# Kernel tuning notes

Hardware: AMD Instinct MI355X
Metric: run time of the kernel (lower is better)

The kernel has to match this reference:

```python
import jax, jax.numpy as jnp
import numpy as np

NUMS = 2048
DIM = 128

def setup_inputs() -> dict:
    key = jax.random.key(0)
    k1, k2 = jax.random.split(key)
    data = jax.random.normal(k1, (32, 512, DIM), dtype=jnp.float32)
    stdv = 1.0 / np.sqrt(DIM)
    weight = jax.random.uniform(k2, (NUMS, DIM), dtype=jnp.float32, minval=-stdv, maxval=stdv)
    return {"data": data, "weight": weight}

def reference(data, weight):
    b, t, d = data.shape
    nums = weight.shape[0]
    # attention scores: [b, t, nums]
    attention = jax.nn.sigmoid(jnp.einsum('btd,kd->btk', data, weight) / jnp.sqrt(jnp.asarray(d, data.dtype)))
    k_top = nums // 16 + 1  # 129
    topk_vals, _ = jax.lax.top_k(attention, k_top)  # [b, t, k_top]
    temporal_att = topk_vals.mean(axis=-1)          # [b, t]
    half = b // 2
    augment = jnp.einsum('btk,kd->btd', attention[:half], weight)  # [b//2, t, d]
    read_query = jnp.concatenate((data[:half], augment), axis=-1)  # [b//2, t, 2d]
    mem_score = 1.0 - temporal_att
    return (mem_score, read_query)
```

## Files before the change

### kernel.cpp

```cpp
#include <hip/hip_runtime.h>

typedef unsigned short u16;
typedef unsigned int u32;
typedef __attribute__((ext_vector_type(8))) short short8;
typedef __attribute__((ext_vector_type(4))) float floatx4;

#define NUMS 2048
#define DIM 128
#define ROWS_TOT 16384
#define HALF_ROWS 8192
#define KTOP 129
#define MTILE 16
#define SP 2056
#define SCALE 0.08838834764831845f

__device__ __forceinline__ u16 f2bf(float f) {
  u32 u = __builtin_bit_cast(u32, f);
  u += 0x7FFFu + ((u >> 16) & 1u);
  return (u16)(u >> 16);
}
__device__ __forceinline__ float bf2f(u32 b) {
  return __builtin_bit_cast(float, b << 16);
}

__global__ void cvt_w_k(const float* __restrict__ w, u16* __restrict__ wb,
                        u16* __restrict__ wt) {
  __shared__ u16 tile[32][33];
  const int tx = threadIdx.x, ty = threadIdx.y;
  const int x = blockIdx.x * 32 + tx;
  const int y0 = blockIdx.y * 32;
#pragma unroll
  for (int j = 0; j < 32; j += 8) {
    const u16 v = f2bf(w[(size_t)(y0 + ty + j) * DIM + x]);
    wb[(size_t)(y0 + ty + j) * DIM + x] = v;
    tile[ty + j][tx] = v;
  }
  __syncthreads();
  const int x2 = y0 + tx;
  const int y2 = blockIdx.x * 32 + ty;
#pragma unroll
  for (int j = 0; j < 32; j += 8)
    wt[(size_t)(y2 + j) * NUMS + x2] = tile[tx][ty + j];
}

__global__ __launch_bounds__(512, 4)
void fused_k(const float* __restrict__ dataF, const u16* __restrict__ wb,
             const u16* __restrict__ wt, float* __restrict__ out) {
  __shared__ u16 S[MTILE * SP];
  const int tid = threadIdx.x;
  const int r0 = blockIdx.x * MTILE;
  const int lane = tid & 63;
  const int wave = tid >> 6;
  const int m = lane & 15;
  const int quad = lane >> 4;

  short8 dfrag[4];
  {
    const float* ap = dataF + (size_t)(r0 + m) * DIM + quad * 8;
#pragma unroll
    for (int ks = 0; ks < 4; ks++) {
      const float4 x = *(const float4*)(ap + ks * 32);
      const float4 y = *(const float4*)(ap + ks * 32 + 4);
      short8 v;
      v[0] = (short)f2bf(x.x); v[1] = (short)f2bf(x.y);
      v[2] = (short)f2bf(x.z); v[3] = (short)f2bf(x.w);
      v[4] = (short)f2bf(y.x); v[5] = (short)f2bf(y.y);
      v[6] = (short)f2bf(y.z); v[7] = (short)f2bf(y.w);
      dfrag[ks] = v;
    }
  }

  u16* sbase = S + m * SP + wave * 256 + quad * 4;
#pragma unroll 4
  for (int nt = 0; nt < 16; nt++) {
    const int n0 = wave * 256 + nt * 16;
    const u16* wp = wb + (size_t)(n0 + m) * DIM + quad * 8;
    floatx4 acc = {0.f, 0.f, 0.f, 0.f};
#pragma unroll
    for (int ks = 0; ks < 4; ks++) {
      const short8 wfrag = *(const short8*)(wp + ks * 32);
      acc = __builtin_amdgcn_mfma_f32_16x16x32_bf16(wfrag, dfrag[ks], acc, 0, 0, 0);
    }
    float a0 = 1.f / (1.f + __expf(-acc[0] * SCALE));
    float a1 = 1.f / (1.f + __expf(-acc[1] * SCALE));
    float a2 = 1.f / (1.f + __expf(-acc[2] * SCALE));
    float a3 = 1.f / (1.f + __expf(-acc[3] * SCALE));
    uint2 p;
    p.x = (u32)f2bf(a0) | ((u32)f2bf(a1) << 16);
    p.y = (u32)f2bf(a2) | ((u32)f2bf(a3) << 16);
    *(uint2*)(sbase + nt * 16) = p;
  }
  __syncthreads();

  if (r0 < HALF_ROWS) {
    {
      const int row = tid >> 5;
      const int c4 = (tid & 31) << 2;
      *(float4*)(out + 16384 + (size_t)(r0 + row) * 256 + c4) =
          *(const float4*)(dataF + (size_t)(r0 + row) * DIM + c4);
    }
    const int n0 = wave * 16;
    const u16* wtp = wt + (size_t)(n0 + m) * NUMS + quad * 8;
    const u16* sp2 = S + m * SP + quad * 8;
    floatx4 acc = {0.f, 0.f, 0.f, 0.f};
#pragma unroll 8
    for (int ks = 0; ks < 64; ks++) {
      const short8 a = *(const short8*)(wtp + ks * 32);
      const short8 b = *(const short8*)(sp2 + ks * 32);
      acc = __builtin_amdgcn_mfma_f32_16x16x32_bf16(a, b, acc, 0, 0, 0);
    }
    float4 st;
    st.x = acc[0]; st.y = acc[1]; st.z = acc[2]; st.w = acc[3];
    *(float4*)(out + 16384 + (size_t)(r0 + m) * 256 + 128 + n0 + quad * 4) = st;
  }

#pragma unroll
  for (int rv = 0; rv < 2; rv++) {
    const int rr = wave * 2 + rv;
    const u16* rp = S + rr * SP + lane * 8;
    u32 x[16], xh[16];
#pragma unroll
    for (int j = 0; j < 4; j++) {
      const short8 v = *(const short8*)(rp + j * 512);
      const u32* pv = (const u32*)&v;
      x[j * 4 + 0] = pv[0]; x[j * 4 + 1] = pv[1];
      x[j * 4 + 2] = pv[2]; x[j * 4 + 3] = pv[3];
    }
#pragma unroll
    for (int i = 0; i < 16; i++) xh[i] = x[i] | 0x80008000u;

    auto cnt_ge = [&](u32 t) -> int {
      const u32 t2 = t * 0x10001u;
      int c = 0;
#pragma unroll
      for (int i = 0; i < 16; i++)
        c += __popc((xh[i] - t2) & 0x80008000u);
      return c;
    };

    int c8[8];
#pragma unroll
    for (int j = 0; j < 8; j++) c8[j] = cnt_ge(0x3F00u + (u32)j);
    u32 pk[4];
#pragma unroll
    for (int j = 0; j < 4; j++) pk[j] = (u32)c8[2 * j] | ((u32)c8[2 * j + 1] << 16);
#pragma unroll
    for (int off = 1; off < 64; off <<= 1) {
#pragma unroll
      for (int j = 0; j < 4; j++) pk[j] += __shfl_xor(pk[j], off);
    }
    int cw[8];
#pragma unroll
    for (int j = 0; j < 4; j++) {
      cw[2 * j] = (int)(pk[j] & 0xFFFFu);
      cw[2 * j + 1] = (int)(pk[j] >> 16);
    }

    u32 lo;
    int cgt;
    if (cw[0] >= KTOP && cw[7] < KTOP) {
      int idx = 0;
#pragma unroll
      for (int j = 1; j < 8; j++) idx += (cw[j] >= KTOP) ? 1 : 0;
      lo = 0x3F00u + (u32)idx;
      cgt = cw[idx + 1];
    } else {
      u32 L = 0u, H = 0x3F81u;
      while (H - L > 1u) {
        const u32 mid = (L + H) >> 1;
        int cc = cnt_ge(mid);
#pragma unroll
        for (int off = 1; off < 64; off <<= 1) cc += __shfl_xor(cc, off);
        if (cc >= KTOP) L = mid; else H = mid;
      }
      lo = L;
      int cg = cnt_ge(lo + 1);
#pragma unroll
      for (int off = 1; off < 64; off <<= 1) cg += __shfl_xor(cg, off);
      cgt = cg;
    }

    const float vstar = bf2f(lo);
    float s = 0.f;
#pragma unroll
    for (int i = 0; i < 16; i++) {
      const float v0 = bf2f(x[i] & 0xFFFFu);
      const float v1 = __builtin_bit_cast(float, x[i] & 0xFFFF0000u);
      if (v0 > vstar) s += v0;
      if (v1 > vstar) s += v1;
    }
#pragma unroll
    for (int off = 1; off < 64; off <<= 1) s += __shfl_xor(s, off);
    if (lane == 0) {
      const float mean = (s + (float)(KTOP - cgt) * vstar) * (1.f / (float)KTOP);
      out[r0 + rr] = 1.f - mean;
    }
  }
}

extern "C" void kernel_launch(void* const* d_in, const int* in_sizes, int n_in,
                              void* d_out, int out_size, void* d_ws, size_t ws_size,
                              hipStream_t stream) {
  const float* data = (const float*)d_in[0];
  const float* weight = (const float*)d_in[1];
  float* out = (float*)d_out;

  u16* wt = (u16*)d_ws;
  u16* wb = wt + NUMS * DIM;

  cvt_w_k<<<dim3(DIM / 32, NUMS / 32), dim3(32, 8), 0, stream>>>(weight, wb, wt);
  fused_k<<<dim3(ROWS_TOT / MTILE), dim3(512), 0, stream>>>(data, wb, wt, out);
}
```

Before: 161.9 us.

## Keep attention tile in registers and split second GEMM across waves

The 16x2048 bf16 attention tile is no longer staged in shared memory. Each wave keeps its 256-column slice in registers. The second GEMM is split along K across the eight waves, with partial sums combined through LDS atomics, and the transposed weight is stored with a permuted column order so that register fragments line up with MFMA operands. The top-k threshold search is reworked into a cooperative count-and-resolve loop over shared counters, and occupancy is raised to 6 blocks per EU. In exchange, it adds LDS atomics, more block-wide syncs per search step, and register pressure from the 32-word register array.

```diff
diff --git a/kernel.cpp b/kernel.cpp
--- a/kernel.cpp
+++ b/kernel.cpp
@@ -4,6 +4,7 @@
 typedef unsigned int u32;
 typedef __attribute__((ext_vector_type(8))) short short8;
 typedef __attribute__((ext_vector_type(4))) float floatx4;
+typedef __attribute__((ext_vector_type(4))) u32 u32x4;
 
 #define NUMS 2048
 #define DIM 128
@@ -11,7 +12,6 @@
 #define HALF_ROWS 8192
 #define KTOP 129
 #define MTILE 16
-#define SP 2056
 #define SCALE 0.08838834764831845f
 
 __device__ __forceinline__ u16 f2bf(float f) {
@@ -36,27 +36,48 @@
     tile[ty + j][tx] = v;
   }
   __syncthreads();
-  const int x2 = y0 + tx;
+  const int k = y0 + tx;
+  const int s = ((k >> 2) & 3) * 8 + ((k >> 4) & 1) * 4 + (k & 3);
+  const int x2p = (k & ~31) | s;
   const int y2 = blockIdx.x * 32 + ty;
 #pragma unroll
   for (int j = 0; j < 32; j += 8)
-    wt[(size_t)(y2 + j) * NUMS + x2] = tile[tx][ty + j];
-}
-
-__global__ __launch_bounds__(512, 4)
+    wt[(size_t)(y2 + j) * NUMS + x2p] = tile[tx][ty + j];
+}
+
+__global__ __launch_bounds__(512, 6)
 void fused_k(const float* __restrict__ dataF, const u16* __restrict__ wb,
              const u16* __restrict__ wt, float* __restrict__ out) {
-  __shared__ u16 S[MTILE * SP];
+  __shared__ floatx4 accb4[16 * 32];
+  __shared__ u32x4 cntb[16][8];
+  __shared__ float vbuf[16];
+  __shared__ u32 cbuf[16];
+  __shared__ u32 basebuf[16];
+  __shared__ float sumbuf[16];
+  __shared__ u32 dbuf[16];
+  __shared__ u32 donecnt;
+  float* const accb = (float*)accb4;
+
   const int tid = threadIdx.x;
   const int r0 = blockIdx.x * MTILE;
   const int lane = tid & 63;
   const int wave = tid >> 6;
   const int m = lane & 15;
   const int quad = lane >> 4;
+  const bool firstHalf = (r0 < HALF_ROWS);
+
+  if (firstHalf) accb4[tid] = (floatx4){0.f, 0.f, 0.f, 0.f};
+  if (tid < 16) {
+    sumbuf[tid] = 0.f;
+    dbuf[tid] = 0u;
+    basebuf[tid] = 0x3F00u;
+  }
+  if (tid == 16) donecnt = 0u;
+  __syncthreads();
 
   short8 dfrag[4];
   {
-    const float* ap = dataF + (size_t)(r0 + m) * DIM + quad * 8;
+    const float* ap = dataF + (r0 + m) * DIM + quad * 8;
 #pragma unroll
     for (int ks = 0; ks < 4; ks++) {
       const float4 x = *(const float4*)(ap + ks * 32);
@@ -70,131 +91,158 @@
     }
   }
 
-  u16* sbase = S + m * SP + wave * 256 + quad * 4;
-#pragma unroll 4
+  u32 patt[32];
+#pragma unroll 2
   for (int nt = 0; nt < 16; nt++) {
     const int n0 = wave * 256 + nt * 16;
-    const u16* wp = wb + (size_t)(n0 + m) * DIM + quad * 8;
+    const u16* wp = wb + (n0 + m) * DIM + quad * 8;
     floatx4 acc = {0.f, 0.f, 0.f, 0.f};
 #pragma unroll
     for (int ks = 0; ks < 4; ks++) {
       const short8 wfrag = *(const short8*)(wp + ks * 32);
       acc = __builtin_amdgcn_mfma_f32_16x16x32_bf16(wfrag, dfrag[ks], acc, 0, 0, 0);
     }
-    float a0 = 1.f / (1.f + __expf(-acc[0] * SCALE));
-    float a1 = 1.f / (1.f + __expf(-acc[1] * SCALE));
-    float a2 = 1.f / (1.f + __expf(-acc[2] * SCALE));
-    float a3 = 1.f / (1.f + __expf(-acc[3] * SCALE));
-    uint2 p;
-    p.x = (u32)f2bf(a0) | ((u32)f2bf(a1) << 16);
-    p.y = (u32)f2bf(a2) | ((u32)f2bf(a3) << 16);
-    *(uint2*)(sbase + nt * 16) = p;
-  }
-  __syncthreads();
-
-  if (r0 < HALF_ROWS) {
+    const float a0 = 1.f / (1.f + __expf(-acc[0] * SCALE));
+    const float a1 = 1.f / (1.f + __expf(-acc[1] * SCALE));
+    const float a2 = 1.f / (1.f + __expf(-acc[2] * SCALE));
+    const float a3 = 1.f / (1.f + __expf(-acc[3] * SCALE));
+    patt[2 * nt] = (u32)f2bf(a0) | ((u32)f2bf(a1) << 16);
+    patt[2 * nt + 1] = (u32)f2bf(a2) | ((u32)f2bf(a3) << 16);
+  }
+
+  if (firstHalf) {
     {
       const int row = tid >> 5;
       const int c4 = (tid & 31) << 2;
       *(float4*)(out + 16384 + (size_t)(r0 + row) * 256 + c4) =
-          *(const float4*)(dataF + (size_t)(r0 + row) * DIM + c4);
-    }
-    const int n0 = wave * 16;
-    const u16* wtp = wt + (size_t)(n0 + m) * NUMS + quad * 8;
-    const u16* sp2 = S + m * SP + quad * 8;
-    floatx4 acc = {0.f, 0.f, 0.f, 0.f};
-#pragma unroll 8
-    for (int ks = 0; ks < 64; ks++) {
-      const short8 a = *(const short8*)(wtp + ks * 32);
-      const short8 b = *(const short8*)(sp2 + ks * 32);
-      acc = __builtin_amdgcn_mfma_f32_16x16x32_bf16(a, b, acc, 0, 0, 0);
-    }
-    float4 st;
-    st.x = acc[0]; st.y = acc[1]; st.z = acc[2]; st.w = acc[3];
-    *(float4*)(out + 16384 + (size_t)(r0 + m) * 256 + 128 + n0 + quad * 4) = st;
-  }
-
-#pragma unroll
-  for (int rv = 0; rv < 2; rv++) {
-    const int rr = wave * 2 + rv;
-    const u16* rp = S + rr * SP + lane * 8;
-    u32 x[16], xh[16];
+          *(const float4*)(dataF + (r0 + row) * DIM + c4);
+    }
+#pragma unroll 1
+    for (int nt2 = 0; nt2 < 8; nt2++) {
+      const u16* wtp = wt + (nt2 * 16 + m) * NUMS + wave * 256 + quad * 8;
+      floatx4 acc = {0.f, 0.f, 0.f, 0.f};
+#pragma unroll
+      for (int ks2 = 0; ks2 < 8; ks2++) {
+        const short8 a = *(const short8*)(wtp + ks2 * 32);
+        const u32x4 bb = {patt[4 * ks2], patt[4 * ks2 + 1],
+                          patt[4 * ks2 + 2], patt[4 * ks2 + 3]};
+        acc = __builtin_amdgcn_mfma_f32_16x16x32_bf16(
+            a, __builtin_bit_cast(short8, bb), acc, 0, 0, 0);
+      }
+#pragma unroll
+      for (int i = 0; i < 4; i++) {
+        const int oc = nt2 * 16 + quad * 4 + i;
+        atomicAdd(accb + m * 128 + (oc ^ m), acc[i]);
+      }
+    }
+  }
+
+  const u32 M8 = 0x80008000u;
+  auto count_pub = [&](u32 base) {
+    u32 pk[4];
 #pragma unroll
     for (int j = 0; j < 4; j++) {
-      const short8 v = *(const short8*)(rp + j * 512);
-      const u32* pv = (const u32*)&v;
-      x[j * 4 + 0] = pv[0]; x[j * 4 + 1] = pv[1];
-      x[j * 4 + 2] = pv[2]; x[j * 4 + 3] = pv[3];
-    }
-#pragma unroll
-    for (int i = 0; i < 16; i++) xh[i] = x[i] | 0x80008000u;
-
-    auto cnt_ge = [&](u32 t) -> int {
-      const u32 t2 = t * 0x10001u;
-      int c = 0;
-#pragma unroll
-      for (int i = 0; i < 16; i++)
-        c += __popc((xh[i] - t2) & 0x80008000u);
-      return c;
-    };
-
-    int c8[8];
-#pragma unroll
-    for (int j = 0; j < 8; j++) c8[j] = cnt_ge(0x3F00u + (u32)j);
-    u32 pk[4];
-#pragma unroll
-    for (int j = 0; j < 4; j++) pk[j] = (u32)c8[2 * j] | ((u32)c8[2 * j + 1] << 16);
-#pragma unroll
-    for (int off = 1; off < 64; off <<= 1) {
-#pragma unroll
-      for (int j = 0; j < 4; j++) pk[j] += __shfl_xor(pk[j], off);
-    }
-    int cw[8];
+      const u32 uA = M8 - (base + 2u * j) * 0x10001u;
+      const u32 uB = uA - 0x10001u;
+      u32 cA = 0, cB = 0;
+#pragma unroll
+      for (int i = 0; i < 32; i++) {
+        cA += __popc((patt[i] + uA) & M8);
+        cB += __popc((patt[i] + uB) & M8);
+      }
+      pk[j] = cA | (cB << 16);
+    }
 #pragma unroll
     for (int j = 0; j < 4; j++) {
-      cw[2 * j] = (int)(pk[j] & 0xFFFFu);
-      cw[2 * j + 1] = (int)(pk[j] >> 16);
-    }
-
-    u32 lo;
-    int cgt;
-    if (cw[0] >= KTOP && cw[7] < KTOP) {
-      int idx = 0;
-#pragma unroll
-      for (int j = 1; j < 8; j++) idx += (cw[j] >= KTOP) ? 1 : 0;
-      lo = 0x3F00u + (u32)idx;
-      cgt = cw[idx + 1];
-    } else {
-      u32 L = 0u, H = 0x3F81u;
-      while (H - L > 1u) {
-        const u32 mid = (L + H) >> 1;
-        int cc = cnt_ge(mid);
-#pragma unroll
-        for (int off = 1; off < 64; off <<= 1) cc += __shfl_xor(cc, off);
-        if (cc >= KTOP) L = mid; else H = mid;
-      }
-      lo = L;
-      int cg = cnt_ge(lo + 1);
-#pragma unroll
-      for (int off = 1; off < 64; off <<= 1) cg += __shfl_xor(cg, off);
-      cgt = cg;
-    }
-
-    const float vstar = bf2f(lo);
+      pk[j] += __shfl_xor(pk[j], 16);
+      pk[j] += __shfl_xor(pk[j], 32);
+    }
+    if (quad == 0)
+      cntb[m][wave ^ (m & 7)] = (u32x4){pk[0], pk[1], pk[2], pk[3]};
+  };
+
+  auto resolve = [&]() {
+    const int rr = wave * 2 + (lane >> 5);
+    if (dbuf[rr]) return;
+    const int L = lane & 31;
+    const u32 base = basebuf[rr];
+    u32x4 c = cntb[rr][(L & 7) ^ (rr & 7)];
+    u32 p0 = c.x, p1 = c.y, p2 = c.z, p3 = c.w;
+#pragma unroll
+    for (int off = 1; off < 8; off <<= 1) {
+      p0 += __shfl_xor(p0, off);
+      p1 += __shfl_xor(p1, off);
+      p2 += __shfl_xor(p2, off);
+      p3 += __shfl_xor(p3, off);
+    }
+    const int cw0 = (int)(p0 & 0xFFFFu), cw1 = (int)(p0 >> 16);
+    const int cw2 = (int)(p1 & 0xFFFFu), cw3 = (int)(p1 >> 16);
+    const int cw4 = (int)(p2 & 0xFFFFu), cw5 = (int)(p2 >> 16);
+    const int cw6 = (int)(p3 & 0xFFFFu), cw7 = (int)(p3 >> 16);
+    if (cw0 >= KTOP && cw7 < KTOP) {
+      const int idx = (cw1 >= KTOP) + (cw2 >= KTOP) + (cw3 >= KTOP) +
+                      (cw4 >= KTOP) + (cw5 >= KTOP) + (cw6 >= KTOP) +
+                      (cw7 >= KTOP);
+      int cgt = 0;
+      cgt = (cw1 < KTOP && cw1 > cgt) ? cw1 : cgt;
+      cgt = (cw2 < KTOP && cw2 > cgt) ? cw2 : cgt;
+      cgt = (cw3 < KTOP && cw3 > cgt) ? cw3 : cgt;
+      cgt = (cw4 < KTOP && cw4 > cgt) ? cw4 : cgt;
+      cgt = (cw5 < KTOP && cw5 > cgt) ? cw5 : cgt;
+      cgt = (cw6 < KTOP && cw6 > cgt) ? cw6 : cgt;
+      cgt = (cw7 < KTOP && cw7 > cgt) ? cw7 : cgt;
+      if (L == 0) {
+        vbuf[rr] = bf2f(base + (u32)idx);
+        cbuf[rr] = (u32)cgt;
+        dbuf[rr] = 1u;
+        atomicAdd(&donecnt, 1u);
+      }
+    } else if (L == 0) {
+      basebuf[rr] = (cw0 < KTOP) ? base - 7u : base + 7u;
+    }
+  };
+
+  count_pub(0x3F00u);
+  __syncthreads();
+  resolve();
+  __syncthreads();
+  while (donecnt < 16u) {
+    count_pub(basebuf[m]);
+    __syncthreads();
+    resolve();
+    __syncthreads();
+  }
+
+  {
+    const float vst = vbuf[m];
     float s = 0.f;
 #pragma unroll
-    for (int i = 0; i < 16; i++) {
-      const float v0 = bf2f(x[i] & 0xFFFFu);
-      const float v1 = __builtin_bit_cast(float, x[i] & 0xFFFF0000u);
-      if (v0 > vstar) s += v0;
-      if (v1 > vstar) s += v1;
-    }
-#pragma unroll
-    for (int off = 1; off < 64; off <<= 1) s += __shfl_xor(s, off);
-    if (lane == 0) {
-      const float mean = (s + (float)(KTOP - cgt) * vstar) * (1.f / (float)KTOP);
-      out[r0 + rr] = 1.f - mean;
-    }
+    for (int i = 0; i < 32; i++) {
+      const float v0 = bf2f(patt[i] & 0xFFFFu);
+      const float v1 = __builtin_bit_cast(float, patt[i] & 0xFFFF0000u);
+      if (v0 > vst) s += v0;
+      if (v1 > vst) s += v1;
+    }
+    s += __shfl_xor(s, 16);
+    s += __shfl_xor(s, 32);
+    if (quad == 0) atomicAdd(&sumbuf[m], s);
+  }
+  __syncthreads();
+
+  if (tid < 16) {
+    const float mean = (sumbuf[tid] + (float)(KTOP - (int)cbuf[tid]) * vbuf[tid]) *
+                       (1.f / (float)KTOP);
+    out[r0 + tid] = 1.f - mean;
+  }
+  if (firstHalf) {
+    const int row = tid >> 5;
+    const int c = tid & 31;
+    const int r = row & 3;
+    floatx4 v = *((floatx4*)(accb + row * 128 + 4 * (c ^ (row >> 2))));
+    if (r & 1) { float t = v[0]; v[0] = v[1]; v[1] = t; t = v[2]; v[2] = v[3]; v[3] = t; }
+    if (r & 2) { float t = v[0]; v[0] = v[2]; v[2] = t; t = v[1]; v[1] = v[3]; v[3] = t; }
+    *(float4*)(out + 16384 + (size_t)(r0 + row) * 256 + 128 + 4 * c) =
+        (float4){v[0], v[1], v[2], v[3]};
   }
 }
 
```

New measurement: 181.1 us. 1.12x slower.
